# Optimization experiments

Hardware: AMD Instinct MI355X
Metric: run time of the kernel (lower is better)

Reference implementation:

```python
import jax, jax.numpy as jnp
import numpy as np

B, T, C = 2, 2048, 1024
NH = 16
HD = C // NH

def setup_inputs() -> dict:
    key = jax.random.key(0)
    k1, k2, k3 = jax.random.split(key, 3)
    x = jax.random.normal(k1, (B, T, C), dtype=jnp.float32)
    w_attn = jax.random.normal(k2, (C, 3 * C), dtype=jnp.float32) * 0.02
    w_proj = jax.random.normal(k3, (C, C), dtype=jnp.float32) * 0.02
    return {"x": x, "w_attn": w_attn, "w_proj": w_proj}

def reference(x, w_attn, w_proj):
    b, t, c = x.shape
    qkv = x @ w_attn                                  # [B,T,3C]
    q, k, v = jnp.split(qkv, 3, axis=-1)
    # [B,NH,T,HD]
    q = q.reshape(b, t, NH, HD).transpose(0, 2, 1, 3)
    k = k.reshape(b, t, NH, HD).transpose(0, 2, 1, 3)
    v = v.reshape(b, t, NH, HD).transpose(0, 2, 1, 3)
    scale = 1.0 / np.sqrt(HD).astype(np.float32)
    att = jnp.einsum('bhqd,bhkd->bhqk', q, k) * scale  # [B,NH,T,T]
    causal = jnp.tril(jnp.ones((t, t), dtype=bool))
    att = jnp.where(causal[None, None], att, jnp.float32(-jnp.inf))
    att = jax.nn.softmax(att, axis=-1)
    y = jnp.einsum('bhqk,bhkd->bhqd', att, v)          # [B,NH,T,HD]
    y = y.transpose(0, 2, 1, 3).reshape(b, t, c)
    return y @ w_proj
```

## Files before the change

### kernel.cpp

```cpp
#include <hip/hip_runtime.h>
#include <hip/hip_bf16.h>

#define BB 2
#define TT 2048
#define CCH 1024
#define NHH 16
#define HDD 64
#define M_TOK (BB*TT)
#define N_QKV (3*CCH)

typedef __attribute__((ext_vector_type(8))) short bf16x8;
typedef __attribute__((ext_vector_type(4))) float f32x4;
typedef unsigned short u16;
typedef unsigned int u32;

__device__ __forceinline__ u16 f2bf(float f) {
    union { float f; u32 u; } v; v.f = f;
    u32 u = v.u;
    u32 r = (u + 0x7FFFu + ((u >> 16) & 1u)) >> 16;
    return (u16)r;
}

__device__ __forceinline__ u32 pk_bf16(float a, float b) {
    u32 ua = __float_as_uint(a) + 0x8000u;
    u32 ub = __float_as_uint(b) + 0x8000u;
    return __builtin_amdgcn_perm(ub, ua, 0x07060302u);
}

__device__ __forceinline__ void async_copy16(const void* g, void* l) {
    __builtin_amdgcn_global_load_lds((__attribute__((address_space(1))) void*)g,
                                     (__attribute__((address_space(3))) void*)l,
                                     16, 0, 0);
}


__global__ __launch_bounds__(256) void cast_bf16_kernel(
    const float* __restrict__ src, u16* __restrict__ dst, int n4) {
    int i = blockIdx.x * 256 + threadIdx.x;
    if (i < n4) {
        float4 f = ((const float4*)src)[i];
        ushort4 o;
        o.x = f2bf(f.x); o.y = f2bf(f.y); o.z = f2bf(f.z); o.w = f2bf(f.w);
        ((ushort4*)dst)[i] = o;
    }
}

__global__ __launch_bounds__(256) void transpose_bf16_kernel(
    const float* __restrict__ src, u16* __restrict__ dst, int R, int Cn,
    int scale_rows, float sc) {
    __shared__ float tile[32][33];
    int c0 = blockIdx.x * 32, r0 = blockIdx.y * 32;
    int tx = threadIdx.x, ty = threadIdx.y;
#pragma unroll
    for (int i = ty; i < 32; i += 8)
        tile[i][tx] = src[(size_t)(r0 + i) * Cn + c0 + tx];
    __syncthreads();
#pragma unroll
    for (int i = ty; i < 32; i += 8) {
        float v = tile[tx][i];
        if (c0 + i < scale_rows) v *= sc;
        dst[(size_t)(c0 + i) * R + r0 + tx] = f2bf(v);
    }
}

__global__ __launch_bounds__(256) void transpose_v_kernel(
    const u16* __restrict__ src, u16* __restrict__ dst) {
    __shared__ u16 tile[32][34];
    int t0 = blockIdx.x * 32, d0 = blockIdx.y * 32, bh = blockIdx.z;
    int tx = threadIdx.x, ty = threadIdx.y;
    const u16* s = src + (size_t)bh * TT * HDD;
    u16* d = dst + (size_t)bh * HDD * TT;
#pragma unroll
    for (int i = ty; i < 32; i += 8)
        tile[i][tx] = s[(size_t)(t0 + i) * HDD + d0 + tx];
    __syncthreads();
#pragma unroll
    for (int i = ty; i < 32; i += 8)
        d[(size_t)(d0 + i) * TT + t0 + tx] = tile[tx][i];
}


__global__ __launch_bounds__(256) void gemm_bt_kernel(
    const u16* __restrict__ A, const u16* __restrict__ Bt,
    int M, int N, int K,
    float* __restrict__ Cout,
    u16* __restrict__ Qo, u16* __restrict__ Ko, u16* __restrict__ Vo,
    int mode)
{
    __shared__ u16 As[128 * 32];
    __shared__ u16 Bs[128 * 32];
    int t = threadIdx.x;
    int m0 = blockIdx.y * 128, n0 = blockIdx.x * 128;
    int lane = t & 63, w = t >> 6;
    int mw = (w >> 1) * 64, nw = (w & 1) * 64;
    int mr = lane & 15, quad = lane >> 4;

    f32x4 zero = {0.f, 0.f, 0.f, 0.f};
    f32x4 acc[4][4];
#pragma unroll
    for (int i = 0; i < 4; ++i)
#pragma unroll
        for (int j = 0; j < 4; ++j) acc[i][j] = zero;

    int rA = t >> 2, ko = (t & 3) << 3;
    const u16* gA0 = A + (size_t)(m0 + rA) * K + ko;
    const u16* gA1 = A + (size_t)(m0 + 64 + rA) * K + ko;
    const u16* gB0 = Bt + (size_t)(n0 + rA) * K + ko;
    const u16* gB1 = Bt + (size_t)(n0 + 64 + rA) * K + ko;
    u16* lA0 = As + (size_t)t * 8;
    u16* lA1 = As + (size_t)(256 + t) * 8;
    u16* lB0 = Bs + (size_t)t * 8;
    u16* lB1 = Bs + (size_t)(256 + t) * 8;

    for (int k0 = 0; k0 < K; k0 += 32) {
        async_copy16(gA0 + k0, lA0);
        async_copy16(gA1 + k0, lA1);
        async_copy16(gB0 + k0, lB0);
        async_copy16(gB1 + k0, lB1);
        __syncthreads();
        bf16x8 af[4], bfr[4];
#pragma unroll
        for (int i = 0; i < 4; ++i)
            af[i] = *(const bf16x8*)&As[(mw + i * 16 + mr) * 32 + quad * 8];
#pragma unroll
        for (int j = 0; j < 4; ++j)
            bfr[j] = *(const bf16x8*)&Bs[(nw + j * 16 + mr) * 32 + quad * 8];
#pragma unroll
        for (int i = 0; i < 4; ++i)
#pragma unroll
            for (int j = 0; j < 4; ++j)
                acc[i][j] = __builtin_amdgcn_mfma_f32_16x16x32_bf16(af[i], bfr[j], acc[i][j], 0, 0, 0);
        __syncthreads();
    }

    if (mode == 0) {
#pragma unroll
        for (int i = 0; i < 4; ++i)
#pragma unroll
            for (int j = 0; j < 4; ++j)
#pragma unroll
                for (int r = 0; r < 4; ++r) {
                    int rg = m0 + mw + i * 16 + quad * 4 + r;
                    int cg = n0 + nw + j * 16 + mr;
                    Cout[(size_t)rg * N + cg] = acc[i][j][r];
                }
    } else {
        int part = n0 >> 10;
        u16* dstp = (part == 0) ? Qo : (part == 1) ? Ko : Vo;
#pragma unroll
        for (int i = 0; i < 4; ++i)
#pragma unroll
            for (int j = 0; j < 4; ++j)
#pragma unroll
                for (int r = 0; r < 4; ++r) {
                    int rg = m0 + mw + i * 16 + quad * 4 + r;
                    int cg = n0 + nw + j * 16 + mr;
                    int cc = cg & 1023;
                    int h = cc >> 6, d = cc & 63;
                    int b = rg >> 11, tt = rg & 2047;
                    int bh = b * NHH + h;
                    dstp[((size_t)bh * TT + tt) * HDD + d] = f2bf(acc[i][j][r]);
                }
    }
}


#define PSTRIDE 72

template<bool MASK>
__device__ __forceinline__ void tile_compute(
    const u16* __restrict__ Ks, const u16* __restrict__ Vs, u16* __restrict__ pb,
    bf16x8 qf0, bf16x8 qf1, int m, int quad, int qcol, int kv0,
    f32x4 (&o)[4], f32x4& ls)
{
    f32x4 zero = {0.f, 0.f, 0.f, 0.f};
    int sw = m & 7;
    f32x4 st[4];
#pragma unroll
    for (int kc = 0; kc < 4; ++kc) {
        int rr = kc * 16 + m;
        bf16x8 kf0 = *(const bf16x8*)&Ks[rr * 64 + ((quad ^ sw) << 3)];
        bf16x8 kf1 = *(const bf16x8*)&Ks[rr * 64 + (((quad + 4) ^ sw) << 3)];
        f32x4 s = __builtin_amdgcn_mfma_f32_16x16x32_bf16(kf0, qf0, zero, 0, 0, 0);
        st[kc]   = __builtin_amdgcn_mfma_f32_16x16x32_bf16(kf1, qf1, s, 0, 0, 0);
    }
#pragma unroll
    for (int kc = 0; kc < 4; ++kc) {
        float e0, e1, e2, e3;
#pragma unroll
        for (int r = 0; r < 4; ++r) {
            float v = st[kc][r];
            if (MASK && (kv0 + kc * 16 + quad * 4 + r > qcol)) v = -1e30f;
            float e = __builtin_amdgcn_exp2f(v);
            ls[r] += e;
            if (r == 0) e0 = e; else if (r == 1) e1 = e; else if (r == 2) e2 = e; else e3 = e;
        }
        uint2 pk; pk.x = pk_bf16(e0, e1); pk.y = pk_bf16(e2, e3);
        *(uint2*)&pb[m * PSTRIDE + kc * 16 + quad * 4] = pk;
    }
#pragma unroll
    for (int ks = 0; ks < 2; ++ks) {
        bf16x8 pf = *(const bf16x8*)&pb[m * PSTRIDE + ks * 32 + quad * 8];
#pragma unroll
        for (int dg = 0; dg < 4; ++dg) {
            int rr = dg * 16 + m;
            bf16x8 vfr = *(const bf16x8*)&Vs[rr * 64 + (((quad + 4 * ks) ^ sw) << 3)];
            o[dg] = __builtin_amdgcn_mfma_f32_16x16x32_bf16(vfr, pf, o[dg], 0, 0, 0);
        }
    }
}

__global__ __launch_bounds__(256) void attn_kernel(
    const u16* __restrict__ Q, const u16* __restrict__ K,
    const u16* __restrict__ Vt, u16* __restrict__ Y)
{
    __shared__ u16 Ks[64 * 64];
    __shared__ u16 Vs[64 * 64];
    __shared__ u16 Pl[4][16 * PSTRIDE];
    int t = threadIdx.x;
    int w = t >> 6, lane = t & 63;
    int m = lane & 15, quad = lane >> 4;

    int bid = blockIdx.x;
    int head = bid & 31;
    int pr = bid >> 5;
    int qbA = pr;
    int qbB = 31 - pr;
    int rowA = qbA * 64 + w * 16;
    int rowB = qbB * 64 + w * 16;

    const u16* qpA = Q + ((size_t)head * TT + rowA + m) * HDD + quad * 8;
    const u16* qpB = Q + ((size_t)head * TT + rowB + m) * HDD + quad * 8;
    bf16x8 qA0 = *(const bf16x8*)qpA;
    bf16x8 qA1 = *(const bf16x8*)(qpA + 32);
    bf16x8 qB0 = *(const bf16x8*)qpB;
    bf16x8 qB1 = *(const bf16x8*)(qpB + 32);

    const u16* kbase = K + (size_t)head * TT * HDD;
    const u16* vbase = Vt + (size_t)head * HDD * TT;
    u16* pb = &Pl[w][0];

    int lr = lane >> 3;
    int cg = (lane & 7) ^ lr;
    int r0 = w * 16 + lr, r1 = r0 + 8;
    u16* ldsK0 = Ks + (size_t)(w * 128 + lane) * 8;
    u16* ldsK1 = Ks + (size_t)(w * 128 + 64 + lane) * 8;
    u16* ldsV0 = Vs + (size_t)(w * 128 + lane) * 8;
    u16* ldsV1 = Vs + (size_t)(w * 128 + 64 + lane) * 8;

    f32x4 zero = {0.f, 0.f, 0.f, 0.f};
    f32x4 oA[4], oB[4], lsA = zero, lsB = zero;
#pragma unroll
    for (int dg = 0; dg < 4; ++dg) { oA[dg] = zero; oB[dg] = zero; }
    int qcolA = rowA + m, qcolB = rowB + m;

    for (int ic = 0; ic <= qbB; ++ic) {
        int kv0 = ic << 6;
        async_copy16(kbase + (size_t)(kv0 + r0) * 64 + cg * 8, ldsK0);
        async_copy16(kbase + (size_t)(kv0 + r1) * 64 + cg * 8, ldsK1);
        async_copy16(vbase + (size_t)r0 * TT + kv0 + cg * 8, ldsV0);
        async_copy16(vbase + (size_t)r1 * TT + kv0 + cg * 8, ldsV1);
        __syncthreads();
        if (ic < qbA)
            tile_compute<false>(Ks, Vs, pb, qA0, qA1, m, quad, qcolA, kv0, oA, lsA);
        else if (ic == qbA)
            tile_compute<true>(Ks, Vs, pb, qA0, qA1, m, quad, qcolA, kv0, oA, lsA);
        if (ic < qbB)
            tile_compute<false>(Ks, Vs, pb, qB0, qB1, m, quad, qcolB, kv0, oB, lsB);
        else
            tile_compute<true>(Ks, Vs, pb, qB0, qB1, m, quad, qcolB, kv0, oB, lsB);
        __syncthreads();
    }

    float lA = (lsA[0] + lsA[1]) + (lsA[2] + lsA[3]);
    float lB = (lsB[0] + lsB[1]) + (lsB[2] + lsB[3]);
    lA += __shfl_xor(lA, 16, 64); lA += __shfl_xor(lA, 32, 64);
    lB += __shfl_xor(lB, 16, 64); lB += __shfl_xor(lB, 32, 64);
    float invA = 1.0f / lA, invB = 1.0f / lB;

    int b = head >> 4, h = head & 15;
    size_t roA = ((size_t)(b * TT + rowA + m)) * CCH + h * HDD;
    size_t roB = ((size_t)(b * TT + rowB + m)) * CCH + h * HDD;
#pragma unroll
    for (int dg = 0; dg < 4; ++dg) {
        uint2 ov;
        ov.x = pk_bf16(oA[dg][0] * invA, oA[dg][1] * invA);
        ov.y = pk_bf16(oA[dg][2] * invA, oA[dg][3] * invA);
        *(uint2*)&Y[roA + dg * 16 + quad * 4] = ov;
        ov.x = pk_bf16(oB[dg][0] * invB, oB[dg][1] * invB);
        ov.y = pk_bf16(oB[dg][2] * invB, oB[dg][3] * invB);
        *(uint2*)&Y[roB + dg * 16 + quad * 4] = ov;
    }
}


extern "C" void kernel_launch(void* const* d_in, const int* in_sizes, int n_in,
                              void* d_out, int out_size, void* d_ws, size_t ws_size,
                              hipStream_t stream) {
    const float* x      = (const float*)d_in[0];
    const float* w_attn = (const float*)d_in[1];
    const float* w_proj = (const float*)d_in[2];
    float* out = (float*)d_out;

    char* ws = (char*)d_ws;
    u16* x_bf   = (u16*)ws; ws += (size_t)M_TOK * CCH * 2;
    u16* wqkvT  = (u16*)ws; ws += (size_t)N_QKV * CCH * 2;
    u16* wprojT = (u16*)ws; ws += (size_t)CCH * CCH * 2;
    u16* qbuf   = (u16*)ws; ws += (size_t)BB * NHH * TT * HDD * 2;
    u16* kbuf   = (u16*)ws; ws += (size_t)BB * NHH * TT * HDD * 2;
    u16* vbuf   = (u16*)ws; ws += (size_t)BB * NHH * TT * HDD * 2;
    u16* vtb    = (u16*)ws; ws += (size_t)BB * NHH * HDD * TT * 2;
    u16* yb     = (u16*)ws; ws += (size_t)M_TOK * CCH * 2;

    const float QSC = 0.125f * 1.44269504088896f;

    cast_bf16_kernel<<<dim3(M_TOK * CCH / 4 / 256), dim3(256), 0, stream>>>(x, x_bf, M_TOK * CCH / 4);
    transpose_bf16_kernel<<<dim3(N_QKV / 32, CCH / 32), dim3(32, 8), 0, stream>>>(
        w_attn, wqkvT, CCH, N_QKV, CCH, QSC);
    transpose_bf16_kernel<<<dim3(CCH / 32, CCH / 32), dim3(32, 8), 0, stream>>>(
        w_proj, wprojT, CCH, CCH, 0, 1.0f);
    gemm_bt_kernel<<<dim3(N_QKV / 128, M_TOK / 128), dim3(256), 0, stream>>>(
        x_bf, wqkvT, M_TOK, N_QKV, CCH, nullptr, qbuf, kbuf, vbuf, 1);
    transpose_v_kernel<<<dim3(TT / 32, HDD / 32, BB * NHH), dim3(32, 8), 0, stream>>>(vbuf, vtb);
    attn_kernel<<<dim3(512), dim3(256), 0, stream>>>(qbuf, kbuf, vtb, yb);
    gemm_bt_kernel<<<dim3(CCH / 128, M_TOK / 128), dim3(256), 0, stream>>>(
        yb, wprojT, M_TOK, CCH, CCH, out, nullptr, nullptr, nullptr, 0);
}
```

Measured before the change: 196.7 us.

## Fuse V transpose into QKV GEMM epilogue and vectorize GEMM stores

Result: slower. 213.5 us (+8.5%).

```diff
diff --git a/kernel.cpp b/kernel.cpp
--- a/kernel.cpp
+++ b/kernel.cpp
@@ -63,34 +63,18 @@
     }
 }
 
-__global__ __launch_bounds__(256) void transpose_v_kernel(
-    const u16* __restrict__ src, u16* __restrict__ dst) {
-    __shared__ u16 tile[32][34];
-    int t0 = blockIdx.x * 32, d0 = blockIdx.y * 32, bh = blockIdx.z;
-    int tx = threadIdx.x, ty = threadIdx.y;
-    const u16* s = src + (size_t)bh * TT * HDD;
-    u16* d = dst + (size_t)bh * HDD * TT;
-#pragma unroll
-    for (int i = ty; i < 32; i += 8)
-        tile[i][tx] = s[(size_t)(t0 + i) * HDD + d0 + tx];
-    __syncthreads();
-#pragma unroll
-    for (int i = ty; i < 32; i += 8)
-        d[(size_t)(d0 + i) * TT + t0 + tx] = tile[tx][i];
-}
-
-
+
+template<int MODE, int SWAP>
 __global__ __launch_bounds__(256) void gemm_bt_kernel(
     const u16* __restrict__ A, const u16* __restrict__ Bt,
-    int M, int N, int K,
+    int M, int N, int K, int n_off,
     float* __restrict__ Cout,
-    u16* __restrict__ Qo, u16* __restrict__ Ko, u16* __restrict__ Vo,
-    int mode)
+    u16* __restrict__ Qo, u16* __restrict__ Ko, u16* __restrict__ Vto)
 {
     __shared__ u16 As[128 * 32];
     __shared__ u16 Bs[128 * 32];
     int t = threadIdx.x;
-    int m0 = blockIdx.y * 128, n0 = blockIdx.x * 128;
+    int m0 = blockIdx.y * 128, n0 = blockIdx.x * 128 + n_off;
     int lane = t & 63, w = t >> 6;
     int mw = (w >> 1) * 64, nw = (w & 1) * 64;
     int mr = lane & 15, quad = lane >> 4;
@@ -128,39 +112,61 @@
 #pragma unroll
         for (int i = 0; i < 4; ++i)
 #pragma unroll
-            for (int j = 0; j < 4; ++j)
-                acc[i][j] = __builtin_amdgcn_mfma_f32_16x16x32_bf16(af[i], bfr[j], acc[i][j], 0, 0, 0);
+            for (int j = 0; j < 4; ++j) {
+                if (SWAP)
+                    acc[i][j] = __builtin_amdgcn_mfma_f32_16x16x32_bf16(bfr[j], af[i], acc[i][j], 0, 0, 0);
+                else
+                    acc[i][j] = __builtin_amdgcn_mfma_f32_16x16x32_bf16(af[i], bfr[j], acc[i][j], 0, 0, 0);
+            }
         __syncthreads();
     }
 
-    if (mode == 0) {
-#pragma unroll
-        for (int i = 0; i < 4; ++i)
-#pragma unroll
-            for (int j = 0; j < 4; ++j)
-#pragma unroll
-                for (int r = 0; r < 4; ++r) {
-                    int rg = m0 + mw + i * 16 + quad * 4 + r;
-                    int cg = n0 + nw + j * 16 + mr;
-                    Cout[(size_t)rg * N + cg] = acc[i][j][r];
-                }
+    if (MODE == 0) {
+#pragma unroll
+        for (int i = 0; i < 4; ++i)
+#pragma unroll
+            for (int j = 0; j < 4; ++j) {
+                int tok = m0 + mw + i * 16 + mr;
+                int cg0 = n0 + nw + j * 16 + quad * 4;
+                float4 v;
+                v.x = acc[i][j][0]; v.y = acc[i][j][1];
+                v.z = acc[i][j][2]; v.w = acc[i][j][3];
+                *(float4*)&Cout[(size_t)tok * N + cg0] = v;
+            }
+    } else if (SWAP == 1) {
+        int part = n0 >> 10;
+        u16* dstp = part ? Ko : Qo;
+#pragma unroll
+        for (int i = 0; i < 4; ++i)
+#pragma unroll
+            for (int j = 0; j < 4; ++j) {
+                int tok = m0 + mw + i * 16 + mr;
+                int cg0 = n0 + nw + j * 16 + quad * 4;
+                int cc = cg0 & 1023;
+                int h = cc >> 6, d0 = cc & 63;
+                int b = tok >> 11, tt = tok & 2047;
+                int bh = b * NHH + h;
+                uint2 o;
+                o.x = pk_bf16(acc[i][j][0], acc[i][j][1]);
+                o.y = pk_bf16(acc[i][j][2], acc[i][j][3]);
+                *(uint2*)&dstp[((size_t)bh * TT + tt) * HDD + d0] = o;
+            }
     } else {
-        int part = n0 >> 10;
-        u16* dstp = (part == 0) ? Qo : (part == 1) ? Ko : Vo;
-#pragma unroll
-        for (int i = 0; i < 4; ++i)
-#pragma unroll
-            for (int j = 0; j < 4; ++j)
-#pragma unroll
-                for (int r = 0; r < 4; ++r) {
-                    int rg = m0 + mw + i * 16 + quad * 4 + r;
-                    int cg = n0 + nw + j * 16 + mr;
-                    int cc = cg & 1023;
-                    int h = cc >> 6, d = cc & 63;
-                    int b = rg >> 11, tt = rg & 2047;
-                    int bh = b * NHH + h;
-                    dstp[((size_t)bh * TT + tt) * HDD + d] = f2bf(acc[i][j][r]);
-                }
+#pragma unroll
+        for (int i = 0; i < 4; ++i)
+#pragma unroll
+            for (int j = 0; j < 4; ++j) {
+                int t0 = m0 + mw + i * 16 + quad * 4;
+                int cg = n0 + nw + j * 16 + mr;
+                int cc = cg & 1023;
+                int h = cc >> 6, d = cc & 63;
+                int b = t0 >> 11, tt0 = t0 & 2047;
+                int bh = b * NHH + h;
+                uint2 o;
+                o.x = pk_bf16(acc[i][j][0], acc[i][j][1]);
+                o.y = pk_bf16(acc[i][j][2], acc[i][j][3]);
+                *(uint2*)&Vto[((size_t)bh * HDD + d) * TT + tt0] = o;
+            }
     }
 }
 
@@ -223,7 +229,8 @@
 
     int bid = blockIdx.x;
     int head = bid & 31;
-    int pr = bid >> 5;
+    int g = bid >> 5;
+    int pr = (g < 8) ? g : 23 - g;
     int qbA = pr;
     int qbB = 31 - pr;
     int rowA = qbA * 64 + w * 16;
@@ -308,7 +315,6 @@
     u16* wprojT = (u16*)ws; ws += (size_t)CCH * CCH * 2;
     u16* qbuf   = (u16*)ws; ws += (size_t)BB * NHH * TT * HDD * 2;
     u16* kbuf   = (u16*)ws; ws += (size_t)BB * NHH * TT * HDD * 2;
-    u16* vbuf   = (u16*)ws; ws += (size_t)BB * NHH * TT * HDD * 2;
     u16* vtb    = (u16*)ws; ws += (size_t)BB * NHH * HDD * TT * 2;
     u16* yb     = (u16*)ws; ws += (size_t)M_TOK * CCH * 2;
 
@@ -319,10 +325,11 @@
         w_attn, wqkvT, CCH, N_QKV, CCH, QSC);
     transpose_bf16_kernel<<<dim3(CCH / 32, CCH / 32), dim3(32, 8), 0, stream>>>(
         w_proj, wprojT, CCH, CCH, 0, 1.0f);
-    gemm_bt_kernel<<<dim3(N_QKV / 128, M_TOK / 128), dim3(256), 0, stream>>>(
-        x_bf, wqkvT, M_TOK, N_QKV, CCH, nullptr, qbuf, kbuf, vbuf, 1);
-    transpose_v_kernel<<<dim3(TT / 32, HDD / 32, BB * NHH), dim3(32, 8), 0, stream>>>(vbuf, vtb);
+    gemm_bt_kernel<1, 1><<<dim3(16, M_TOK / 128), dim3(256), 0, stream>>>(
+        x_bf, wqkvT, M_TOK, N_QKV, CCH, 0, nullptr, qbuf, kbuf, nullptr);
+    gemm_bt_kernel<1, 0><<<dim3(8, M_TOK / 128), dim3(256), 0, stream>>>(
+        x_bf, wqkvT, M_TOK, N_QKV, CCH, 2048, nullptr, nullptr, nullptr, vtb);
     attn_kernel<<<dim3(512), dim3(256), 0, stream>>>(qbuf, kbuf, vtb, yb);
-    gemm_bt_kernel<<<dim3(CCH / 128, M_TOK / 128), dim3(256), 0, stream>>>(
-        yb, wprojT, M_TOK, CCH, CCH, out, nullptr, nullptr, nullptr, 0);
-}
+    gemm_bt_kernel<0, 1><<<dim3(8, M_TOK / 128), dim3(256), 0, stream>>>(
+        yb, wprojT, M_TOK, CCH, CCH, 0, out, nullptr, nullptr, nullptr);
+}
```
